# Optimization experiments

Measured on AMD Instinct MI355X. Metric: run time of the kernel, lower is better.

## Reference

```python
import jax, jax.numpy as jnp
import numpy as np

DN = ('NCH', 'OIH', 'NCH')


def _dsc(x, dwk, dwb, pwk, pwb, groups):
    # depthwise conv (VALID) + pointwise 1x1 conv, both with bias
    y = jax.lax.conv_general_dilated(x, dwk, (1,), 'VALID', dimension_numbers=DN,
                                     feature_group_count=groups) + dwb[None, :, None]
    y = jax.lax.conv_general_dilated(y, pwk, (1,), 'VALID', dimension_numbers=DN) + pwb[None, :, None]
    return y


def _icoh(x):
    # x: (b, c, L) -> iCOH adjacency (b, c, c)
    b, c, _ = x.shape
    f = jnp.fft.fft(x, axis=-1)                                  # (b,c,L) complex
    cps = f[:, :, None, :] * jnp.conj(f)[:, None, :, :]          # (b,c,c,L)
    num = jnp.mean(jnp.imag(cps), axis=-1)
    den = jnp.sqrt(jnp.mean(jnp.abs(cps), axis=-1) ** 2)
    adj = num / den
    return (adj * (1.0 - jnp.eye(c, dtype=adj.dtype))).astype(jnp.float32)


def _forward(x, se_w1, se_w2, dw_k1, dw_b1, pw_k1, pw_b1, dw_k2, dw_b2, pw_k2, pw_b2,
             dw_k3, dw_b3, pw_k3, pw_b3, gcn_w, gcn_b,
             w_r, wb_r, w_u, wb_u, w_c, wb_c, b_r, b_u, b_c):
    b, s, c, L = x.shape
    out_gru = w_r.shape[1]
    # Squeeze-and-Excitation over segment dim, then max over segments
    sq = x.mean(axis=(2, 3))                                     # (b,s)
    a = jax.nn.sigmoid(jax.nn.relu(sq @ se_w1) @ se_w2)          # (b,s)
    max_seg = (x * a[:, :, None, None]).max(axis=1)              # (b,c,L)
    adj = _icoh(max_seg)                                         # (b,c,c)

    def step(h, xt):                                             # h: (b*c,gru), xt: (b,c,L)
        d = _dsc(xt, dw_k1, dw_b1, pw_k1, pw_b1, c)
        d = _dsc(d, dw_k2, dw_b2, pw_k2, pw_b2, c)
        d = _dsc(d, dw_k3, dw_b3, pw_k3, pw_b3, c)               # (b,c,c)
        adj_t = jax.nn.sigmoid(d + adj)
        g = (jnp.einsum('bij,bjl->bil', adj_t, xt) @ gcn_w + gcn_b).reshape(b * c, -1)
        cat = jnp.concatenate([g, h], axis=-1)
        r = jax.nn.sigmoid(cat @ w_r + wb_r + b_r)
        u = jax.nn.sigmoid(cat @ w_u + wb_u + b_u)
        ct = jnp.tanh(jnp.concatenate([g, r * h], axis=-1) @ w_c + wb_c + b_c)
        h = u * h + (1.0 - u) * ct
        return h, None

    h0 = jnp.zeros((b * c, out_gru), x.dtype)
    hT, _ = jax.lax.scan(step, h0, jnp.swapaxes(x, 0, 1))        # scan over s
    return hT.reshape(b, c, out_gru)[:, -1, :]                   # (b, out_gru)


def setup_inputs():
    key = jax.random.key(0)
    b, s, c, L, gcn, gru = 64, 30, 62, 169, 64, 64
    ks = jax.random.split(key, 16)
    W = 0.05
    inp = {
        'x': jax.random.normal(ks[0], (b, s, c, L), jnp.float32),
        'se_w1': jax.random.normal(ks[1], (s, s // 2), jnp.float32) * W,
        'se_w2': jax.random.normal(ks[2], (s // 2, s), jnp.float32) * W,
        'dw_k1': jax.random.normal(ks[3], (c, 1, 64), jnp.float32) * W,
        'dw_b1': jnp.zeros((c,), jnp.float32),
        'pw_k1': jax.random.normal(ks[4], (c, c, 1), jnp.float32) * W,
        'pw_b1': jnp.zeros((c,), jnp.float32),
        'dw_k2': jax.random.normal(ks[5], (c, 1, 32), jnp.float32) * W,
        'dw_b2': jnp.zeros((c,), jnp.float32),
        'pw_k2': jax.random.normal(ks[6], (c, c, 1), jnp.float32) * W,
        'pw_b2': jnp.zeros((c,), jnp.float32),
        'dw_k3': jax.random.normal(ks[7], (c, 1, 14), jnp.float32) * W,
        'dw_b3': jnp.zeros((c,), jnp.float32),
        'pw_k3': jax.random.normal(ks[8], (c, c, 1), jnp.float32) * W,
        'pw_b3': jnp.zeros((c,), jnp.float32),
        'gcn_w': jax.random.normal(ks[9], (L, gcn), jnp.float32) * W,
        'gcn_b': jnp.zeros((gcn,), jnp.float32),
        'w_r': jax.random.normal(ks[10], (gcn + gru, gru), jnp.float32) * W,
        'wb_r': jnp.zeros((gru,), jnp.float32),
        'w_u': jax.random.normal(ks[11], (gcn + gru, gru), jnp.float32) * W,
        'wb_u': jnp.zeros((gru,), jnp.float32),
        'w_c': jax.random.normal(ks[12], (gcn + gru, gru), jnp.float32) * W,
        'wb_c': jnp.zeros((gru,), jnp.float32),
        'b_r': jnp.zeros((gru,), jnp.float32),
        'b_u': jnp.zeros((gru,), jnp.float32),
        'b_c': jnp.zeros((gru,), jnp.float32),
    }
    return inp


def reference(x, se_w1, se_w2, dw_k1, dw_b1, pw_k1, pw_b1, dw_k2, dw_b2, pw_k2, pw_b2,
              dw_k3, dw_b3, pw_k3, pw_b3, gcn_w, gcn_b,
              w_r, wb_r, w_u, wb_u, w_c, wb_c, b_r, b_u, b_c):
    return _forward(x, se_w1, se_w2, dw_k1, dw_b1, pw_k1, pw_b1, dw_k2, dw_b2, pw_k2, pw_b2,
                    dw_k3, dw_b3, pw_k3, pw_b3, gcn_w, gcn_b,
                    w_r, wb_r, w_u, wb_u, w_c, wb_c, b_r, b_u, b_c)
```

## Files before the change

### kernel.cpp

```cpp
#include <hip/hip_runtime.h>
#include <hip/hip_bf16.h>
#include <math.h>

#define Bb 64
#define Ss 30
#define Cc 62
#define Ll 169
#define CL (Cc*Ll)
#define GRU 64
#define HTAPS 108
#define KSPLIT 32
#define NTILES 164
#define HBS 10496

typedef __attribute__((ext_vector_type(8))) short short8;
typedef __attribute__((ext_vector_type(4))) float f32x4;

__device__ __forceinline__ unsigned short f2bf(float f)
{
    union { float f; unsigned int u; } v; v.f = f;
    unsigned int u = v.u + 0x7fffu + ((v.u >> 16) & 1u);
    return (unsigned short)(u >> 16);
}


__global__ __launch_bounds__(256) void k_prep(
    const float* __restrict__ dwk1, const float* __restrict__ dwb1,
    const float* __restrict__ pwk1, const float* __restrict__ pwb1,
    const float* __restrict__ dwk2, const float* __restrict__ dwb2,
    const float* __restrict__ pwk2, const float* __restrict__ pwb2,
    const float* __restrict__ dwk3, const float* __restrict__ dwb3,
    const float* __restrict__ pwk3, const float* __restrict__ pwb3,
    float* __restrict__ Ccst, unsigned short* __restrict__ HBt)
{
    const int c = blockIdx.x, t = threadIdx.x;
    if (c == Cc) {
        for (int u = t; u < 64*(HBS - CL); u += 256) {
            int j = u / (HBS - CL), l = u % (HBS - CL);
            HBt[(size_t)j*HBS + CL + l] = 0;
        }
        __shared__ float s0[Cc], s1[Cc], s2[Cc];
        if (t < Cc) s0[t] = dwb1[t];
        __syncthreads();
        if (t < Cc) {
            float acc = pwb1[t];
            for (int cc2 = 0; cc2 < Cc; ++cc2) acc += pwk1[t*Cc + cc2] * s0[cc2];
            float sk = 0.f;
            for (int a = 0; a < 32; ++a) sk += dwk2[t*32 + a];
            s1[t] = acc * sk + dwb2[t];
        }
        __syncthreads();
        if (t < Cc) {
            float acc = pwb2[t];
            for (int e = 0; e < Cc; ++e) acc += pwk2[t*Cc + e] * s1[e];
            float sk = 0.f;
            for (int tt = 0; tt < 14; ++tt) sk += dwk3[t*14 + tt];
            s2[t] = acc * sk + dwb3[t];
        }
        __syncthreads();
        if (t < 64) {
            float v = (t < Cc) ? pwk3[61*Cc + t] * s2[t] : 0.f;
            for (int off = 32; off; off >>= 1) v += __shfl_down(v, off);
            if (t == 0) Ccst[0] = v + pwb3[61];
        }
        return;
    }
    __shared__ float q[Cc];
    __shared__ float F[Cc*14];
    __shared__ float G[Cc*45];
    __shared__ float H1[45], hc[HTAPS];
    if (t < Cc) q[t] = pwk3[61*Cc + t];
    __syncthreads();
    for (int u = t; u < Cc*14; u += 256) {
        int e = u / 14, tt = u % 14;
        float acc = 0.f;
        for (int f = 0; f < Cc; ++f) acc += q[f] * pwk2[f*Cc + e] * dwk3[f*14 + tt];
        F[u] = acc;
    }
    __syncthreads();
    for (int u = t; u < Cc*45; u += 256) {
        int e = u / 45, s = u % 45;
        float acc = 0.f;
        int t0 = s - 31; if (t0 < 0) t0 = 0;
        int t1 = s; if (t1 > 13) t1 = 13;
        for (int tt = t0; tt <= t1; ++tt) acc += F[e*14 + tt] * dwk2[e*32 + (s - tt)];
        G[u] = acc;
    }
    __syncthreads();
    if (t < 45) {
        float acc = 0.f;
        for (int e = 0; e < Cc; ++e) acc += pwk1[e*Cc + c] * G[e*45 + t];
        H1[t] = acc;
    }
    __syncthreads();
    if (t < HTAPS) {
        float acc = 0.f;
        int s0 = t - 63; if (s0 < 0) s0 = 0;
        int s1 = t; if (s1 > 44) s1 = 44;
        for (int s = s0; s <= s1; ++s) acc += H1[s] * dwk1[c*64 + (t - s)];
        hc[t] = acc;
    }
    __syncthreads();
    for (int u = t; u < 64*Ll; u += 256) {
        int j = u / Ll, l = u - j*Ll;
        int a = l - j;
        unsigned short v = 0;
        if (a >= 0 && a < HTAPS) v = f2bf(hc[a]);
        HBt[(size_t)j*HBS + c*Ll + l] = v;
    }
}

__global__ __launch_bounds__(256) void k_gemm(const float* __restrict__ x,
                                              const unsigned short* __restrict__ HBt,
                                              float* __restrict__ P)
{
    __shared__ __align__(16) unsigned short Xs[64*64];
    __shared__ __align__(16) unsigned short Hs[64*64];
    const int tid = threadIdx.x;
    const int mt = blockIdx.x % 30;
    const int ks = blockIdx.x / 30;
    const int t0 = (NTILES * ks) / KSPLIT;
    const int t1 = (NTILES * (ks + 1)) / KSPLIT;
    const int m0g = mt * 64;
    const int w = tid >> 6, l = tid & 63;
    const int arow = w*16 + (l & 15);
    const int klane = (l >> 4) * 8;
    const int sr = tid >> 2, sq4 = (tid & 3) << 4;

    f32x4 acc[4];
#pragma unroll
    for (int ct = 0; ct < 4; ++ct) acc[ct] = (f32x4){0.f, 0.f, 0.f, 0.f};

    for (int kt = t0; kt < t1; ++kt) {
        const int kb = kt * 64;
        {
            const float* xp = x + (size_t)(m0g + sr)*CL + kb + sq4;
            unsigned short tb[16];
            if (kb + 64 <= CL) {
#pragma unroll
                for (int t2 = 0; t2 < 8; ++t2) {
                    float2 v = *reinterpret_cast<const float2*>(xp + 2*t2);
                    tb[2*t2]   = f2bf(v.x);
                    tb[2*t2+1] = f2bf(v.y);
                }
            } else {
#pragma unroll
                for (int t = 0; t < 16; ++t) {
                    int col = kb + sq4 + t;
                    tb[t] = f2bf((col < CL) ? xp[t] : 0.f);
                }
            }
            int i0 = (sr*64 + sq4)     ^ ((sr & 7) << 3);
            int i1 = (sr*64 + sq4 + 8) ^ ((sr & 7) << 3);
            short8 p0, p1;
#pragma unroll
            for (int t = 0; t < 8; ++t) { p0[t] = (short)tb[t]; p1[t] = (short)tb[t+8]; }
            *reinterpret_cast<short8*>(&Xs[i0]) = p0;
            *reinterpret_cast<short8*>(&Xs[i1]) = p1;
        }
        {
            const unsigned short* hp = HBt + (size_t)sr*HBS + kb + sq4;
            short8 p0 = *reinterpret_cast<const short8*>(hp);
            short8 p1 = *reinterpret_cast<const short8*>(hp + 8);
            int i0 = (sr*64 + sq4)     ^ ((sr & 7) << 3);
            int i1 = (sr*64 + sq4 + 8) ^ ((sr & 7) << 3);
            *reinterpret_cast<short8*>(&Hs[i0]) = p0;
            *reinterpret_cast<short8*>(&Hs[i1]) = p1;
        }
        __syncthreads();
#pragma unroll
        for (int ks2 = 0; ks2 < 2; ++ks2) {
            int kk0 = ks2*32 + klane;
            int ia = (arow*64 + kk0) ^ ((arow & 7) << 3);
            short8 af = *reinterpret_cast<const short8*>(&Xs[ia]);
#pragma unroll
            for (int ct = 0; ct < 4; ++ct) {
                int bcol = ct*16 + (l & 15);
                int ib = (bcol*64 + kk0) ^ ((bcol & 7) << 3);
                short8 bf = *reinterpret_cast<const short8*>(&Hs[ib]);
                acc[ct] = __builtin_amdgcn_mfma_f32_16x16x32_bf16(af, bf, acc[ct], 0, 0, 0);
            }
        }
        __syncthreads();
    }
#pragma unroll
    for (int ct = 0; ct < 4; ++ct) {
        int col = ct*16 + (l & 15);
        if (col < Cc) {
#pragma unroll
            for (int i = 0; i < 4; ++i) {
                int row = m0g + w*16 + (l >> 4)*4 + i;
                P[(size_t)(ks*1920 + row)*Cc + col] = acc[ct][i];
            }
        }
    }
}

__global__ __launch_bounds__(256) void k_g(const float* __restrict__ x, const float* __restrict__ P,
    const float* __restrict__ Ccst,
    const float* __restrict__ gcn_w, const float* __restrict__ gcn_b,
    const float* __restrict__ w_r, const float* __restrict__ w_u, const float* __restrict__ w_c,
    float* __restrict__ preR, float* __restrict__ preU, float* __restrict__ preC)
{
    __shared__ float adjt[Cc];
    __shared__ float v[Ll];
    __shared__ float g[GRU];
    int bt = blockIdx.x, t = bt >> 6, b = bt & 63;
    int m = b * Ss + t;
    int tid = threadIdx.x;
    if (tid < Cc) {
        float sv = Ccst[0];
#pragma unroll
        for (int ks = 0; ks < KSPLIT; ++ks) sv += P[((size_t)ks*1920 + m)*Cc + tid];
        adjt[tid] = 1.f / (1.f + expf(-sv));
    }
    __syncthreads();
    if (tid < Ll) {
        const float* xp = x + (size_t)m*CL + tid;
        float acc = 0.f;
        for (int j = 0; j < Cc; ++j) acc += adjt[j] * xp[j*Ll];
        v[tid] = acc;
    }
    __syncthreads();
    if (tid < GRU) {
        float acc = gcn_b[tid];
        for (int l = 0; l < Ll; ++l) acc += v[l] * gcn_w[l*GRU + tid];
        g[tid] = acc;
    }
    __syncthreads();
    if (tid < GRU) {
        float ar = 0.f, au = 0.f, ac = 0.f;
        for (int i = 0; i < GRU; ++i) {
            float gi = g[i];
            ar += gi * w_r[i*GRU + tid];
            au += gi * w_u[i*GRU + tid];
            ac += gi * w_c[i*GRU + tid];
        }
        preR[(size_t)bt*GRU + tid] = ar;
        preU[(size_t)bt*GRU + tid] = au;
        preC[(size_t)bt*GRU + tid] = ac;
    }
}

__global__ __launch_bounds__(256) void k_gru(const float* __restrict__ preR, const float* __restrict__ preU,
    const float* __restrict__ preC,
    const float* __restrict__ w_r, const float* __restrict__ wb_r,
    const float* __restrict__ w_u, const float* __restrict__ wb_u,
    const float* __restrict__ w_c, const float* __restrict__ wb_c,
    const float* __restrict__ b_r, const float* __restrict__ b_u, const float* __restrict__ b_c,
    float* __restrict__ out)
{
    __shared__ float h[GRU], rh[GRU];
    __shared__ float part[3][4][GRU];
    __shared__ float preS[Ss][3][GRU];
    const int b = blockIdx.x;
    const int t = threadIdx.x, o = t & 63, q = t >> 6;

    float wr[16], wu[16], wc[16];
#pragma unroll
    for (int i = 0; i < 16; ++i) {
        wr[i] = w_r[(GRU + q*16 + i)*GRU + o];
        wu[i] = w_u[(GRU + q*16 + i)*GRU + o];
        wc[i] = w_c[(GRU + q*16 + i)*GRU + o];
    }
    for (int u = t; u < Ss*GRU; u += 256) {
        int s = u >> 6, oo = u & 63;
        size_t base = (size_t)(s*Bb + b)*GRU + oo;
        preS[s][0][oo] = preR[base];
        preS[s][1][oo] = preU[base];
        preS[s][2][oo] = preC[base];
    }
    const float cr = wb_r[o] + b_r[o];
    const float cu = wb_u[o] + b_u[o];
    const float cc = wb_c[o] + b_c[o];
    if (t < GRU) h[t] = 0.f;
    float ug = 0.f;
    __syncthreads();

    for (int s = 0; s < Ss; ++s) {
        float ar = 0.f, au = 0.f;
#pragma unroll
        for (int i = 0; i < 16; ++i) {
            float hi = h[q*16 + i];
            ar += hi * wr[i];
            au += hi * wu[i];
        }
        part[0][q][o] = ar;
        part[1][q][o] = au;
        __syncthreads();
        if (q == 0) {
            float arf = preS[s][0][o] + cr + part[0][0][o] + part[0][1][o] + part[0][2][o] + part[0][3][o];
            float auf = preS[s][1][o] + cu + part[1][0][o] + part[1][1][o] + part[1][2][o] + part[1][3][o];
            float r = 1.f / (1.f + expf(-arf));
            ug = 1.f / (1.f + expf(-auf));
            rh[o] = r * h[o];
        }
        __syncthreads();
        float ac = 0.f;
#pragma unroll
        for (int i = 0; i < 16; ++i) ac += rh[q*16 + i] * wc[i];
        part[2][q][o] = ac;
        __syncthreads();
        if (q == 0) {
            float acf = preS[s][2][o] + cc + part[2][0][o] + part[2][1][o] + part[2][2][o] + part[2][3][o];
            float ct = tanhf(acf);
            float hn = ug * h[o] + (1.f - ug) * ct;
            h[o] = hn;
            if (s == Ss - 1) out[b*GRU + o] = hn;
        }
        __syncthreads();
    }
}

extern "C" void kernel_launch(void* const* d_in, const int* in_sizes, int n_in,
                              void* d_out, int out_size, void* d_ws, size_t ws_size,
                              hipStream_t stream)
{
    const float* x     = (const float*)d_in[0];
    const float* dwk1  = (const float*)d_in[3];
    const float* dwb1  = (const float*)d_in[4];
    const float* pwk1  = (const float*)d_in[5];
    const float* pwb1  = (const float*)d_in[6];
    const float* dwk2  = (const float*)d_in[7];
    const float* dwb2  = (const float*)d_in[8];
    const float* pwk2  = (const float*)d_in[9];
    const float* pwb2  = (const float*)d_in[10];
    const float* dwk3  = (const float*)d_in[11];
    const float* dwb3  = (const float*)d_in[12];
    const float* pwk3  = (const float*)d_in[13];
    const float* pwb3  = (const float*)d_in[14];
    const float* gcn_w = (const float*)d_in[15];
    const float* gcn_b = (const float*)d_in[16];
    const float* w_r   = (const float*)d_in[17];
    const float* wb_r  = (const float*)d_in[18];
    const float* w_u   = (const float*)d_in[19];
    const float* wb_u  = (const float*)d_in[20];
    const float* w_c   = (const float*)d_in[21];
    const float* wb_c  = (const float*)d_in[22];
    const float* b_r   = (const float*)d_in[23];
    const float* b_u   = (const float*)d_in[24];
    const float* b_c   = (const float*)d_in[25];
    float* out = (float*)d_out;

    float* ws   = (float*)d_ws;
    float* P    = ws;
    float* preR = P    + 3809280;
    float* preU = preR + 122880;
    float* preC = preU + 122880;
    float* Ccst = preC + 122880;
    unsigned short* HBt = (unsigned short*)(Ccst + 8);

    k_prep<<<Cc + 1, 256, 0, stream>>>(dwk1, dwb1, pwk1, pwb1, dwk2, dwb2, pwk2, pwb2,
                                       dwk3, dwb3, pwk3, pwb3, Ccst, HBt);
    k_gemm<<<30*KSPLIT, 256, 0, stream>>>(x, HBt, P);
    k_g<<<Ss*Bb, 256, 0, stream>>>(x, P, Ccst, gcn_w, gcn_b, w_r, w_u, w_c, preR, preU, preC);
    k_gru<<<Bb, 256, 0, stream>>>(preR, preU, preC, w_r, wb_r, w_u, wb_u, w_c, wb_c,
                                  b_r, b_u, b_c, out);
}
```

Before: 106.5 us.

## Split weight-prep into two kernels and halve GEMM K-split count

The old prep kernel had every one of the 62 blocks recompute the full F and G intermediates (Cc*14 and Cc*45 reductions). That work is now computed once, spread across blocks in a new k_misc kernel, and written to a global buffer that a second kernel, k_h1h, reads to build the banded H matrix. Separately, KSPLIT drops from 32 to 16, halving the GEMM grid and the partial-sum buffer P. This removes redundant prep work and shrinks the P traffic that k_g reduces, at the cost of one extra kernel launch and fewer GEMM blocks.

New measurement: 87.37 us. -18.0%, faster.

```diff
diff --git a/kernel.cpp b/kernel.cpp
--- a/kernel.cpp
+++ b/kernel.cpp
@@ -9,7 +9,7 @@
 #define CL (Cc*Ll)
 #define GRU 64
 #define HTAPS 108
-#define KSPLIT 32
+#define KSPLIT 16
 #define NTILES 164
 #define HBS 10496
 
@@ -24,27 +24,40 @@
 }
 
 
-__global__ __launch_bounds__(256) void k_prep(
-    const float* __restrict__ dwk1, const float* __restrict__ dwb1,
-    const float* __restrict__ pwk1, const float* __restrict__ pwb1,
+__global__ __launch_bounds__(256) void k_misc(
+    const float* __restrict__ pwk1, const float* __restrict__ pwb1, const float* __restrict__ dwb1,
     const float* __restrict__ dwk2, const float* __restrict__ dwb2,
     const float* __restrict__ pwk2, const float* __restrict__ pwb2,
     const float* __restrict__ dwk3, const float* __restrict__ dwb3,
     const float* __restrict__ pwk3, const float* __restrict__ pwb3,
-    float* __restrict__ Ccst, unsigned short* __restrict__ HBt)
-{
-    const int c = blockIdx.x, t = threadIdx.x;
-    if (c == Cc) {
-        for (int u = t; u < 64*(HBS - CL); u += 256) {
-            int j = u / (HBS - CL), l = u % (HBS - CL);
-            HBt[(size_t)j*HBS + CL + l] = 0;
-        }
-        __shared__ float s0[Cc], s1[Cc], s2[Cc];
+    float* __restrict__ Gout, float* __restrict__ Ccst)
+{
+    __shared__ float s0[Cc], s1[Cc], s2[Cc], F[14], k2[32];
+    const int blk = blockIdx.x, t = threadIdx.x;
+    if (blk < Cc) {
+        const int e = blk;
+        if (t < Cc) { s0[t] = pwk3[61*Cc + t]; s1[t] = pwk2[t*Cc + e]; }
+        if (t < 32) k2[t] = dwk2[e*32 + t];
+        __syncthreads();
+        if (t < 14) {
+            float acc = 0.f;
+            for (int f = 0; f < Cc; ++f) acc += s0[f] * s1[f] * dwk3[f*14 + t];
+            F[t] = acc;
+        }
+        __syncthreads();
+        if (t < 45) {
+            float acc = 0.f;
+            int t0 = t - 31; if (t0 < 0) t0 = 0;
+            int t1 = t; if (t1 > 13) t1 = 13;
+            for (int tt = t0; tt <= t1; ++tt) acc += F[tt] * k2[t - tt];
+            Gout[e*45 + t] = acc;
+        }
+    } else {
         if (t < Cc) s0[t] = dwb1[t];
         __syncthreads();
         if (t < Cc) {
             float acc = pwb1[t];
-            for (int cc2 = 0; cc2 < Cc; ++cc2) acc += pwk1[t*Cc + cc2] * s0[cc2];
+            for (int c = 0; c < Cc; ++c) acc += pwk1[t*Cc + c] * s0[c];
             float sk = 0.f;
             for (int a = 0; a < 32; ++a) sk += dwk2[t*32 + a];
             s1[t] = acc * sk + dwb2[t];
@@ -63,33 +76,28 @@
             for (int off = 32; off; off >>= 1) v += __shfl_down(v, off);
             if (t == 0) Ccst[0] = v + pwb3[61];
         }
+    }
+}
+
+__global__ __launch_bounds__(256) void k_h1h(const float* __restrict__ pwk1, const float* __restrict__ dwk1,
+                                             const float* __restrict__ Gin,
+                                             unsigned short* __restrict__ HBt)
+{
+    const int c = blockIdx.x, t = threadIdx.x;
+    if (c == Cc) {
+        for (int u = t; u < 64*(HBS - CL); u += 256) {
+            int j = u / (HBS - CL), l = u % (HBS - CL);
+            HBt[(size_t)j*HBS + CL + l] = 0;
+        }
         return;
     }
-    __shared__ float q[Cc];
-    __shared__ float F[Cc*14];
-    __shared__ float G[Cc*45];
-    __shared__ float H1[45], hc[HTAPS];
-    if (t < Cc) q[t] = pwk3[61*Cc + t];
-    __syncthreads();
-    for (int u = t; u < Cc*14; u += 256) {
-        int e = u / 14, tt = u % 14;
-        float acc = 0.f;
-        for (int f = 0; f < Cc; ++f) acc += q[f] * pwk2[f*Cc + e] * dwk3[f*14 + tt];
-        F[u] = acc;
-    }
-    __syncthreads();
-    for (int u = t; u < Cc*45; u += 256) {
-        int e = u / 45, s = u % 45;
-        float acc = 0.f;
-        int t0 = s - 31; if (t0 < 0) t0 = 0;
-        int t1 = s; if (t1 > 13) t1 = 13;
-        for (int tt = t0; tt <= t1; ++tt) acc += F[e*14 + tt] * dwk2[e*32 + (s - tt)];
-        G[u] = acc;
-    }
+    __shared__ float p1c[Cc], H1[45], k1[64], hc[HTAPS];
+    if (t < Cc) p1c[t] = pwk1[t*Cc + c];
+    if (t >= 64 && t < 128) k1[t - 64] = dwk1[c*64 + (t - 64)];
     __syncthreads();
     if (t < 45) {
         float acc = 0.f;
-        for (int e = 0; e < Cc; ++e) acc += pwk1[e*Cc + c] * G[e*45 + t];
+        for (int e = 0; e < Cc; ++e) acc += p1c[e] * Gin[e*45 + t];
         H1[t] = acc;
     }
     __syncthreads();
@@ -97,7 +105,7 @@
         float acc = 0.f;
         int s0 = t - 63; if (s0 < 0) s0 = 0;
         int s1 = t; if (s1 > 44) s1 = 44;
-        for (int s = s0; s <= s1; ++s) acc += H1[s] * dwk1[c*64 + (t - s)];
+        for (int s = s0; s <= s1; ++s) acc += H1[s] * k1[t - s];
         hc[t] = acc;
     }
     __syncthreads();
@@ -344,14 +352,16 @@
 
     float* ws   = (float*)d_ws;
     float* P    = ws;
-    float* preR = P    + 3809280;
+    float* preR = P    + 1904640;
     float* preU = preR + 122880;
     float* preC = preU + 122880;
     float* Ccst = preC + 122880;
-    unsigned short* HBt = (unsigned short*)(Ccst + 8);
-
-    k_prep<<<Cc + 1, 256, 0, stream>>>(dwk1, dwb1, pwk1, pwb1, dwk2, dwb2, pwk2, pwb2,
-                                       dwk3, dwb3, pwk3, pwb3, Ccst, HBt);
+    float* Gbuf = Ccst + 8;
+    unsigned short* HBt = (unsigned short*)(Gbuf + 2790);
+
+    k_misc<<<Cc + 1, 256, 0, stream>>>(pwk1, pwb1, dwb1, dwk2, dwb2, pwk2, pwb2,
+                                       dwk3, dwb3, pwk3, pwb3, Gbuf, Ccst);
+    k_h1h<<<Cc + 1, 256, 0, stream>>>(pwk1, dwk1, Gbuf, HBt);
     k_gemm<<<30*KSPLIT, 256, 0, stream>>>(x, HBt, P);
     k_g<<<Ss*Bb, 256, 0, stream>>>(x, P, Ccst, gcn_w, gcn_b, w_r, w_u, w_c, preR, preU, preC);
     k_gru<<<Bb, 256, 0, stream>>>(preR, preU, preC, w_r, wb_r, w_u, wb_u, w_c, wb_c,
```
